# Performance work log

Measured on AMD Instinct MI355X. Metric: run time of the kernel, lower is better.

The kernel has to match this reference:

```python
import jax, jax.numpy as jnp
import numpy as np

N_NODES, N_EDGES, N_FEAT, DIM, HEADS, N_PRED, N_CLASS, N_STEPS = 10000, 160000, 64, 64, 4, 2, 16, 4


def setup_inputs() -> dict:
    key = jax.random.key(0)
    ks = jax.random.split(key, 16)
    def lin(k, fi, fo):
        return jax.random.normal(k, (fi, fo), jnp.float32) / np.sqrt(fi)
    return {
        "x": jax.random.normal(ks[0], (N_NODES, N_FEAT), jnp.float32),
        "edge_index": jax.random.randint(ks[1], (2, N_EDGES), 0, N_NODES, jnp.int64),
        "enc_W": lin(ks[2], N_FEAT, DIM), "enc_b": jnp.zeros((DIM,), jnp.float32),
        "gat_Wl": lin(ks[3], DIM, HEADS * DIM), "gat_bl": jnp.zeros((HEADS * DIM,), jnp.float32),
        "gat_Wr": lin(ks[4], DIM, HEADS * DIM), "gat_br": jnp.zeros((HEADS * DIM,), jnp.float32),
        "gat_att": jax.random.normal(ks[5], (HEADS, DIM), jnp.float32) / np.sqrt(DIM),
        "gat_bias": jnp.zeros((HEADS * DIM,), jnp.float32),
        "W1": lin(ks[6], HEADS * DIM, DIM), "b1": jnp.zeros((DIM,), jnp.float32),
        "W2": lin(ks[7], DIM, DIM), "b2": jnp.zeros((DIM,), jnp.float32),
        "act_W": lin(ks[8], DIM, 1), "act_b": jnp.zeros((1,), jnp.float32),
        "dec_W": jax.random.normal(ks[9], (N_PRED, DIM, N_CLASS), jnp.float32) / np.sqrt(DIM),
        "dec_b": jnp.zeros((N_PRED, N_CLASS), jnp.float32),
        "num_steps": N_STEPS,
    }


def reference(x, edge_index, enc_W, enc_b, gat_Wl, gat_bl, gat_Wr, gat_br,
              gat_att, gat_bias, W1, b1, W2, b2, act_W, act_b, dec_W, dec_b, num_steps):
    N = x.shape[0]
    H, C = gat_att.shape  # heads, per-head channels
    # PyG GATv2Conv adds self-loops by default
    loops = jnp.arange(N, dtype=edge_index.dtype)
    src = jnp.concatenate([edge_index[0], loops])
    dst = jnp.concatenate([edge_index[1], loops])

    h0 = x @ enc_W + enc_b  # encoder

    def step(carry, _):
        h, total, final = carry
        # GATv2: per-edge score on lin_l(src) + lin_r(dst)
        xl = (h @ gat_Wl + gat_bl).reshape(N, H, C)
        xr = (h @ gat_Wr + gat_br).reshape(N, H, C)
        e = jax.nn.leaky_relu(xl[src] + xr[dst], 0.2)          # [E, H, C]
        logits = jnp.einsum('ehc,hc->eh', e, gat_att)           # [E, H]
        m = jax.ops.segment_max(logits, dst, num_segments=N)    # segment softmax over dst
        ex = jnp.exp(logits - m[dst])
        denom = jax.ops.segment_sum(ex, dst, num_segments=N)
        alpha = ex / (denom[dst] + 1e-16)
        agg = jax.ops.segment_sum(xl[src] * alpha[:, :, None], dst, num_segments=N)
        g = agg.reshape(N, H * C) + gat_bias                    # concat heads + bias
        hn = jax.nn.relu(g @ W1 + b1) @ W2 + b2                 # process2 MLP
        # ACT halting: weighted accumulation, deltas clipped so weights sum to <= 1
        term = jax.nn.sigmoid(hn @ act_W + act_b)               # [N, 1]
        new_total = jnp.minimum(total + term, 1.0)
        delta = jnp.minimum(term, new_total - total)
        return (hn, total + delta, final + delta * hn), None

    carry0 = (h0, jnp.zeros((N, 1), x.dtype), jnp.zeros((N, h0.shape[1]), x.dtype))
    (_, _, final), _ = jax.lax.scan(step, carry0, None, length=num_steps)

    logits = jnp.einsum('nd,pdc->pnc', final, dec_W) + dec_b[:, None, :]
    return jax.nn.log_softmax(logits, axis=-1)  # [num_predictions, N, num_classes]
```

## Files before the change

kernel.cpp:

```cpp
#include <hip/hip_runtime.h>
#include <hip/hip_bf16.h>
#include <hip/hip_fp16.h>

#define N_NODES 10000
#define N_EDGES 160000
#define N_E2    (N_EDGES + N_NODES)
#define DIM     64
#define HD      256
#define N_PRED  2
#define N_CLASS 16
#define N_STEPS 4

typedef __hip_bfloat16 bf16;
__device__ __forceinline__ float b2f(bf16 v) { return __bfloat162float(v); }
__device__ __forceinline__ int clampn(int v) { return v < 0 ? 0 : (v >= N_NODES ? N_NODES - 1 : v); }

typedef _Float16 h2_t __attribute__((ext_vector_type(2)));

__device__ __forceinline__ float dot2(unsigned int a, unsigned int b, float c) {
#if __has_builtin(__builtin_amdgcn_fdot2)
    h2_t av, bv;
    __builtin_memcpy(&av, &a, 4);
    __builtin_memcpy(&bv, &b, 4);
    return __builtin_amdgcn_fdot2(av, bv, c, false);
#else
    __half2 ah = *(__half2*)&a, bh = *(__half2*)&b;
    float2 af = __half22float2(ah), bf = __half22float2(bh);
    return c + af.x * bf.x + af.y * bf.y;
#endif
}

struct ConvTable {
    const void* src[17];
    int start[18];
};

__global__ void detect_kernel(const unsigned int* __restrict__ e32,
                              const unsigned short* __restrict__ x16,
                              int* __restrict__ flags) {
    __shared__ int ce, cf;
    if (threadIdx.x == 0) { ce = 0; cf = 0; }
    __syncthreads();
    int le = 0;
    for (int i = threadIdx.x; i < 2048; i += 256)
        le += (e32[2 * i + 1] != 0u) ? 1 : 0;
    int lf = 0;
    for (int i = threadIdx.x; i < 1024; i += 256) {
        unsigned short u = x16[2 * i];
        int ex = (u >> 7) & 0xFF;
        lf += (u == 0 || (ex >= 114 && ex <= 141)) ? 1 : 0;
    }
    atomicAdd(&ce, le);
    atomicAdd(&cf, lf);
    __syncthreads();
    if (threadIdx.x == 0) {
        flags[0] = (ce < 1024) ? 1 : 0;
        flags[1] = (cf >= 512) ? 1 : 0;
    }
}

__global__ void convert_kernel(ConvTable tab, const int* __restrict__ flags,
                               float* __restrict__ xf) {
    int i = blockIdx.x * 256 + threadIdx.x;
    if (i >= tab.start[17]) return;
    int j = 0;
    #pragma unroll
    for (int k = 1; k < 17; ++k) j += (i >= tab.start[k]) ? 1 : 0;
    int off = i - tab.start[j];
    float v;
    if (flags[1]) v = b2f(((const bf16*)tab.src[j])[off]);
    else          v = ((const float*)tab.src[j])[off];
    xf[i] = v;
}

__global__ void pack_kernel(const float* __restrict__ xf,
                            int oWl, int oWr, int oW1, int oW2,
                            __half* __restrict__ wp) {
    int i = blockIdx.x * 256 + threadIdx.x;
    if (i >= 26624) return;
    int base, width, loc;
    if (i < 8192)       { loc = i;         base = oWl; width = 256; }
    else if (i < 16384) { loc = i - 8192;  base = oWr; width = 256; }
    else if (i < 24576) { loc = i - 16384; base = oW1; width = 64; }
    else                { loc = i - 24576; base = oW2; width = 64; }
    int k2 = loc / width, c = loc % width;
    wp[2 * i]     = __float2half(xf[base + (2 * k2) * width + c]);
    wp[2 * i + 1] = __float2half(xf[base + (2 * k2 + 1) * width + c]);
}

__global__ void hist_kernel(const int* __restrict__ edges, const int* __restrict__ flags,
                            int* __restrict__ deg) {
    int e = blockIdx.x * 256 + threadIdx.x;
    if (e >= N_E2) return;
    int i64 = flags[0];
    int dst;
    if (e < N_EDGES) dst = clampn(i64 ? edges[2 * (N_EDGES + e)] : edges[N_EDGES + e]);
    else             dst = e - N_EDGES;
    atomicAdd(&deg[dst], 1);
}

__global__ void scan_kernel(const int* __restrict__ deg, int* __restrict__ off) {
    __shared__ int partial[1024];
    const int tid = threadIdx.x;
    const int per = (N_NODES + 1023) / 1024;
    int local[16];
    int base = tid * per;
    int s = 0;
    for (int i = 0; i < per; ++i) {
        int v = (base + i < N_NODES) ? deg[base + i] : 0;
        local[i] = s;
        s += v;
    }
    partial[tid] = s;
    __syncthreads();
    for (int d = 1; d < 1024; d <<= 1) {
        int t = (tid >= d) ? partial[tid - d] : 0;
        __syncthreads();
        partial[tid] += t;
        __syncthreads();
    }
    int offset = (tid > 0) ? partial[tid - 1] : 0;
    for (int i = 0; i < per; ++i)
        if (base + i < N_NODES) off[base + i] = offset + local[i];
    if (tid == 1023) off[N_NODES] = partial[1023];
}

__global__ void scatter_kernel(const int* __restrict__ edges, const int* __restrict__ flags,
                               const int* __restrict__ off, int* __restrict__ cursor,
                               int* __restrict__ csr_src) {
    int e = blockIdx.x * 256 + threadIdx.x;
    if (e >= N_E2) return;
    int i64 = flags[0];
    int src, dst;
    if (e < N_EDGES) {
        src = clampn(i64 ? edges[2 * e] : edges[e]);
        dst = clampn(i64 ? edges[2 * (N_EDGES + e)] : edges[N_EDGES + e]);
    } else { src = dst = e - N_EDGES; }
    int pos = off[dst] + atomicAdd(&cursor[dst], 1);
    csr_src[pos] = src;
}

__global__ __launch_bounds__(256) void enc_proj_kernel(
        const float* __restrict__ Xf,
        const float* __restrict__ encW, const float* __restrict__ encB,
        const float* __restrict__ Wl, const float* __restrict__ bl,
        const float* __restrict__ Wr, const float* __restrict__ br,
        __half* __restrict__ xlh, float* __restrict__ xr) {
    __shared__ float xs[8][DIM];
    __shared__ float h0[8][DIM];
    const int t = threadIdx.x, pp = t >> 6, d = t & 63;
    const int n0 = blockIdx.x * 8;
    ((float*)xs)[t]       = Xf[n0 * DIM + t];
    ((float*)xs)[t + 256] = Xf[n0 * DIM + t + 256];
    __syncthreads();
    float ah0 = encB[d], ah1 = encB[d];
    for (int k = 0; k < DIM; ++k) {
        float wv = encW[k * DIM + d];
        ah0 += xs[pp][k] * wv;
        ah1 += xs[pp + 4][k] * wv;
    }
    h0[pp][d]     = ah0;
    h0[pp + 4][d] = ah1;
    __syncthreads();
    float al[8] = {0,0,0,0,0,0,0,0}, ar[8] = {0,0,0,0,0,0,0,0};
    for (int k = 0; k < DIM; ++k) {
        float wl = Wl[k * HD + t], wr = Wr[k * HD + t];
        #pragma unroll
        for (int j = 0; j < 8; ++j) { al[j] += h0[j][k] * wl; ar[j] += h0[j][k] * wr; }
    }
    float bbl = bl[t], bbr = br[t];
    #pragma unroll
    for (int j = 0; j < 8; ++j) {
        xlh[(size_t)(n0 + j) * HD + t] = __float2half(al[j] + bbl);
        xr[(size_t)(n0 + j) * HD + t] = ar[j] + bbr;
    }
}

__global__ __launch_bounds__(256) void edge_agg_kernel(
        const __half* __restrict__ xlh, const float* __restrict__ xr,
        const float* __restrict__ att, const float* __restrict__ gbias,
        const int* __restrict__ off, const int* __restrict__ csr_src,
        __half* __restrict__ gbufh) {
    __shared__ float red_m[4][4];
    __shared__ float red_s[4][4];
    __shared__ float red_acc[4][HD];
    const int n = blockIdx.x;
    const int t = threadIdx.x, w = t >> 6, l = t & 63;
    const int e0 = off[n], e1 = off[n + 1];
    const float4 xr4 = ((const float4*)(xr + (size_t)n * HD))[l];
    const float4 at4 = ((const float4*)att)[l];

    float m = -1e30f, s = 0.f;
    float4 acc = {0.f, 0.f, 0.f, 0.f};
    const uint2 zero2 = {0u, 0u};
    int e = e0 + w;
    uint2 b0 = zero2, b1v = zero2, b2v = zero2, b3v = zero2;
    if (e < e1)      b0  = ((const uint2*)(xlh + (size_t)csr_src[e] * HD))[l];
    if (e + 4 < e1)  b1v = ((const uint2*)(xlh + (size_t)csr_src[e + 4] * HD))[l];
    if (e + 8 < e1)  b2v = ((const uint2*)(xlh + (size_t)csr_src[e + 8] * HD))[l];
    if (e + 12 < e1) b3v = ((const uint2*)(xlh + (size_t)csr_src[e + 12] * HD))[l];
    for (; e < e1; e += 4) {
        uint2 cur = b0;
        b0 = b1v; b1v = b2v; b2v = b3v;
        if (e + 16 < e1)
            b3v = ((const uint2*)(xlh + (size_t)csr_src[e + 16] * HD))[l];
        __half2 h01 = *reinterpret_cast<__half2*>(&cur.x);
        __half2 h23 = *reinterpret_cast<__half2*>(&cur.y);
        float2 f01 = __half22float2(h01);
        float2 f23 = __half22float2(h23);
        float c0 = f01.x, c1 = f01.y, c2 = f23.x, c3 = f23.y;
        float z0 = c0 + xr4.x, z1 = c1 + xr4.y, z2 = c2 + xr4.z, z3 = c3 + xr4.w;
        z0 = (z0 > 0.f) ? z0 : 0.2f * z0;
        z1 = (z1 > 0.f) ? z1 : 0.2f * z1;
        z2 = (z2 > 0.f) ? z2 : 0.2f * z2;
        z3 = (z3 > 0.f) ? z3 : 0.2f * z3;
        float p = z0 * at4.x + z1 * at4.y + z2 * at4.z + z3 * at4.w;
        #pragma unroll
        for (int mo = 8; mo; mo >>= 1) p += __shfl_xor(p, mo, 64);
        float nm = fmaxf(m, p);
        float sc = __expf(m - nm);
        float wv = __expf(p - nm);
        s = s * sc + wv;
        acc.x = acc.x * sc + wv * c0;
        acc.y = acc.y * sc + wv * c1;
        acc.z = acc.z * sc + wv * c2;
        acc.w = acc.w * sc + wv * c3;
        m = nm;
    }
    if ((l & 15) == 0) { red_m[w][l >> 4] = m; red_s[w][l >> 4] = s; }
    ((float4*)red_acc[w])[l] = acc;
    __syncthreads();
    {
        int hh = t >> 6;
        float m0 = red_m[0][hh], m1 = red_m[1][hh], m2 = red_m[2][hh], m3 = red_m[3][hh];
        float mm = fmaxf(fmaxf(m0, m1), fmaxf(m2, m3));
        float f0 = __expf(m0 - mm), f1 = __expf(m1 - mm),
              f2 = __expf(m2 - mm), f3 = __expf(m3 - mm);
        float ss = red_s[0][hh] * f0 + red_s[1][hh] * f1 +
                   red_s[2][hh] * f2 + red_s[3][hh] * f3;
        float aa = red_acc[0][t] * f0 + red_acc[1][t] * f1 +
                   red_acc[2][t] * f2 + red_acc[3][t] * f3;
        gbufh[(size_t)n * HD + t] = __float2half(aa / (ss + 1e-16f) + gbias[t]);
    }
}

__global__ __launch_bounds__(256) void mlp_act_proj_kernel(
        const __half* __restrict__ gbufh, const __half* __restrict__ wp,
        const float* __restrict__ b1, const float* __restrict__ b2,
        const float* __restrict__ actW, const float* __restrict__ actB,
        const float* __restrict__ bl, const float* __restrict__ br,
        float* __restrict__ act_tot, float* __restrict__ final_,
        __half* __restrict__ xlh, float* __restrict__ xr, int do_proj) {
    __shared__ unsigned int gall_u[4][128];
    __shared__ float part[4][HD];
    __shared__ __half us_h[4][DIM];
    __shared__ float hns[4][DIM];
    __shared__ __half hns_h[4][DIM];
    __shared__ float delta[4];
    const int t = threadIdx.x, pp = t >> 6, d = t & 63;
    const int n0 = blockIdx.x * 4;

    const unsigned int* Wlp = (const unsigned int*)wp;
    const unsigned int* Wrp = Wlp + 8192;
    const unsigned int* W1p = Wlp + 16384;
    const unsigned int* W2p = Wlp + 24576;

    {
        const unsigned int* gb = (const unsigned int*)gbufh;
        ((unsigned int*)gall_u)[t]       = gb[(size_t)n0 * 128 + t];
        ((unsigned int*)gall_u)[t + 256] = gb[(size_t)n0 * 128 + t + 256];
    }
    __syncthreads();

    {
        float acc[4] = {0.f, 0.f, 0.f, 0.f};
        for (int k2 = pp * 32; k2 < pp * 32 + 32; ++k2) {
            unsigned int w2 = W1p[k2 * 64 + d];
            #pragma unroll
            for (int j = 0; j < 4; ++j) acc[j] = dot2(gall_u[j][k2], w2, acc[j]);
        }
        #pragma unroll
        for (int j = 0; j < 4; ++j) part[j][t] = acc[j];
    }
    __syncthreads();
    {
        float v = part[pp][d] + part[pp][64 + d] + part[pp][128 + d] + part[pp][192 + d] + b1[d];
        us_h[pp][d] = __float2half(fmaxf(v, 0.f));
    }
    __syncthreads();

    {
        const unsigned int* us_u = (const unsigned int*)us_h;
        float acc[4] = {0.f, 0.f, 0.f, 0.f};
        for (int k2 = pp * 8; k2 < pp * 8 + 8; ++k2) {
            unsigned int w2 = W2p[k2 * 64 + d];
            #pragma unroll
            for (int j = 0; j < 4; ++j) acc[j] = dot2(us_u[j * 32 + k2], w2, acc[j]);
        }
        #pragma unroll
        for (int j = 0; j < 4; ++j) part[j][t] = acc[j];
    }
    __syncthreads();
    {
        float hv = part[pp][d] + part[pp][64 + d] + part[pp][128 + d] + part[pp][192 + d] + b2[d];
        hns[pp][d] = hv;
        hns_h[pp][d] = __float2half(hv);
    }
    __syncthreads();

    {
        float p = hns[pp][d] * actW[d];
        #pragma unroll
        for (int mo = 32; mo; mo >>= 1) p += __shfl_xor(p, mo, 64);
        if (d == 0) {
            float term = 1.f / (1.f + __expf(-(p + actB[0])));
            float tot = act_tot[n0 + pp];
            float nt = fminf(tot + term, 1.f);
            float dl = fminf(term, nt - tot);
            act_tot[n0 + pp] = tot + dl;
            delta[pp] = dl;
        }
    }
    __syncthreads();
    final_[(size_t)(n0 + pp) * DIM + d] += delta[pp] * hns[pp][d];

    if (do_proj) {
        const unsigned int* hn_u = (const unsigned int*)hns_h;
        float al[4] = {0.f, 0.f, 0.f, 0.f}, ar[4] = {0.f, 0.f, 0.f, 0.f};
        for (int k2 = 0; k2 < 32; ++k2) {
            unsigned int wl2 = Wlp[k2 * 256 + t];
            unsigned int wr2 = Wrp[k2 * 256 + t];
            #pragma unroll
            for (int j = 0; j < 4; ++j) {
                unsigned int hh = hn_u[j * 32 + k2];
                al[j] = dot2(hh, wl2, al[j]);
                ar[j] = dot2(hh, wr2, ar[j]);
            }
        }
        float bbl = bl[t], bbr = br[t];
        #pragma unroll
        for (int j = 0; j < 4; ++j) {
            xlh[(size_t)(n0 + j) * HD + t] = __float2half(al[j] + bbl);
            xr[(size_t)(n0 + j) * HD + t] = ar[j] + bbr;
        }
    }
}

__global__ void decoder_kernel(const float* __restrict__ final_,
                               const float* __restrict__ decW, const float* __restrict__ decB,
                               const int* __restrict__ flags, void* __restrict__ outv) {
    int id = blockIdx.x * 256 + threadIdx.x;
    if (id >= N_NODES * N_PRED * N_CLASS) return;
    int n = id >> 5, r = id & 31, p = r >> 4, c = r & 15;
    float acc = decB[p * N_CLASS + c];
    for (int dd = 0; dd < DIM; ++dd)
        acc += final_[(size_t)n * DIM + dd] * decW[(p * DIM + dd) * N_CLASS + c];
    float mx = acc;
    #pragma unroll
    for (int mo = 8; mo; mo >>= 1) mx = fmaxf(mx, __shfl_xor(mx, mo, 64));
    float ex = __expf(acc - mx);
    float ss = ex;
    #pragma unroll
    for (int mo = 8; mo; mo >>= 1) ss += __shfl_xor(ss, mo, 64);
    float ov = acc - mx - logf(ss);
    int oi = p * (N_NODES * N_CLASS) + n * N_CLASS + c;
    if (flags[1]) ((bf16*)outv)[oi] = __float2bfloat16(ov);
    else          ((float*)outv)[oi] = ov;
}

static size_t align256(size_t x) { return (x + 255) & ~size_t(255); }

extern "C" void kernel_launch(void* const* d_in, const int* in_sizes, int n_in,
                              void* d_out, int out_size, void* d_ws, size_t ws_size,
                              hipStream_t stream) {
    const int* edges = (const int*)d_in[1];

    static const int fids[17] = {0, 2, 3, 4, 5, 6, 7, 8, 9, 10, 11, 12, 13, 14, 15, 16, 17};
    ConvTable tab;
    int cum = 0;
    for (int i = 0; i < 17; ++i) {
        tab.src[i] = d_in[fids[i]];
        tab.start[i] = cum;
        cum += in_sizes[fids[i]];
    }
    tab.start[17] = cum;

    char* w = (char*)d_ws;
    size_t o = 0;
    int* flags     = (int*)(w + o); o = align256(o + 16 * sizeof(int));
    int* off       = (int*)(w + o); o = align256(o + (N_NODES + 1) * sizeof(int));
    size_t zbase = o;
    int* deg       = (int*)(w + o); o = align256(o + N_NODES * sizeof(int));
    int* cursor    = (int*)(w + o); o = align256(o + N_NODES * sizeof(int));
    float* act_tot = (float*)(w + o); o = align256(o + N_NODES * sizeof(float));
    float* final_  = (float*)(w + o); o = align256(o + (size_t)N_NODES * DIM * sizeof(float));
    size_t zsize = o - zbase;
    int* csr_src   = (int*)(w + o); o = align256(o + N_E2 * sizeof(int));
    float* xf      = (float*)(w + o); o = align256(o + (size_t)cum * sizeof(float));
    __half* xlh    = (__half*)(w + o); o = align256(o + (size_t)N_NODES * HD * sizeof(__half));
    float* xr      = (float*)(w + o); o = align256(o + (size_t)N_NODES * HD * sizeof(float));
    __half* gbufh  = (__half*)(w + o); o = align256(o + (size_t)N_NODES * HD * sizeof(__half));
    __half* wpack  = (__half*)(w + o); o = align256(o + 53248 * sizeof(__half));
    if (o > ws_size) return;

    const float* Xf   = xf + tab.start[0];
    const float* encW = xf + tab.start[1];
    const float* encB = xf + tab.start[2];
    const float* Wl   = xf + tab.start[3];
    const float* bl   = xf + tab.start[4];
    const float* Wr   = xf + tab.start[5];
    const float* br   = xf + tab.start[6];
    const float* att  = xf + tab.start[7];
    const float* gbias= xf + tab.start[8];
    const float* b1   = xf + tab.start[10];
    const float* b2   = xf + tab.start[12];
    const float* actW = xf + tab.start[13];
    const float* actB = xf + tab.start[14];
    const float* decW = xf + tab.start[15];
    const float* decB = xf + tab.start[16];

    hipMemsetAsync(w + zbase, 0, zsize, stream);

    detect_kernel<<<1, 256, 0, stream>>>((const unsigned int*)d_in[1],
                                         (const unsigned short*)d_in[0], flags);
    convert_kernel<<<(cum + 255) / 256, 256, 0, stream>>>(tab, flags, xf);
    pack_kernel<<<(26624 + 255) / 256, 256, 0, stream>>>(
        xf, tab.start[3], tab.start[5], tab.start[9], tab.start[11], wpack);

    int eb = (N_E2 + 255) / 256;
    hist_kernel<<<eb, 256, 0, stream>>>(edges, flags, deg);
    scan_kernel<<<1, 1024, 0, stream>>>(deg, off);
    scatter_kernel<<<eb, 256, 0, stream>>>(edges, flags, off, cursor, csr_src);

    enc_proj_kernel<<<N_NODES / 8, 256, 0, stream>>>(Xf, encW, encB, Wl, bl, Wr, br, xlh, xr);

    for (int step = 0; step < N_STEPS; ++step) {
        edge_agg_kernel<<<N_NODES, 256, 0, stream>>>(xlh, xr, att, gbias, off, csr_src, gbufh);
        mlp_act_proj_kernel<<<N_NODES / 4, 256, 0, stream>>>(
            gbufh, wpack, b1, b2, actW, actB, bl, br,
            act_tot, final_, xlh, xr, (step < N_STEPS - 1) ? 1 : 0);
    }

    int db = (N_NODES * N_PRED * N_CLASS + 255) / 256;
    decoder_kernel<<<db, 256, 0, stream>>>(final_, decW, decB, flags, d_out);
}
```

Before: 338.9 us.

## Map one wavefront per destination node in GAT edge aggregation

Each 64-lane wavefront now owns a whole destination node and walks all of its incoming edges, instead of four wavefronts splitting one node's edges. This removes the LDS cross-wave softmax merge and the block barrier, and the grid shrinks to a quarter of the blocks. Source rows are prefetched in groups of four, with clamped indices and masking for invalid edges, to keep several gathers in flight. In exchange, each wave handles a longer serial edge chain and some redundant loads of the last edge occur at group tails.

```diff
diff --git a/kernel.cpp b/kernel.cpp
--- a/kernel.cpp
+++ b/kernel.cpp
@@ -181,67 +181,65 @@
         const float* __restrict__ att, const float* __restrict__ gbias,
         const int* __restrict__ off, const int* __restrict__ csr_src,
         __half* __restrict__ gbufh) {
-    __shared__ float red_m[4][4];
-    __shared__ float red_s[4][4];
-    __shared__ float red_acc[4][HD];
-    const int n = blockIdx.x;
     const int t = threadIdx.x, w = t >> 6, l = t & 63;
+    const int n = blockIdx.x * 4 + w;
     const int e0 = off[n], e1 = off[n + 1];
+    const int elast = e1 - 1;
     const float4 xr4 = ((const float4*)(xr + (size_t)n * HD))[l];
     const float4 at4 = ((const float4*)att)[l];
 
     float m = -1e30f, s = 0.f;
     float4 acc = {0.f, 0.f, 0.f, 0.f};
-    const uint2 zero2 = {0u, 0u};
-    int e = e0 + w;
-    uint2 b0 = zero2, b1v = zero2, b2v = zero2, b3v = zero2;
-    if (e < e1)      b0  = ((const uint2*)(xlh + (size_t)csr_src[e] * HD))[l];
-    if (e + 4 < e1)  b1v = ((const uint2*)(xlh + (size_t)csr_src[e + 4] * HD))[l];
-    if (e + 8 < e1)  b2v = ((const uint2*)(xlh + (size_t)csr_src[e + 8] * HD))[l];
-    if (e + 12 < e1) b3v = ((const uint2*)(xlh + (size_t)csr_src[e + 12] * HD))[l];
-    for (; e < e1; e += 4) {
-        uint2 cur = b0;
-        b0 = b1v; b1v = b2v; b2v = b3v;
-        if (e + 16 < e1)
-            b3v = ((const uint2*)(xlh + (size_t)csr_src[e + 16] * HD))[l];
-        __half2 h01 = *reinterpret_cast<__half2*>(&cur.x);
-        __half2 h23 = *reinterpret_cast<__half2*>(&cur.y);
-        float2 f01 = __half22float2(h01);
-        float2 f23 = __half22float2(h23);
-        float c0 = f01.x, c1 = f01.y, c2 = f23.x, c3 = f23.y;
-        float z0 = c0 + xr4.x, z1 = c1 + xr4.y, z2 = c2 + xr4.z, z3 = c3 + xr4.w;
-        z0 = (z0 > 0.f) ? z0 : 0.2f * z0;
-        z1 = (z1 > 0.f) ? z1 : 0.2f * z1;
-        z2 = (z2 > 0.f) ? z2 : 0.2f * z2;
-        z3 = (z3 > 0.f) ? z3 : 0.2f * z3;
-        float p = z0 * at4.x + z1 * at4.y + z2 * at4.z + z3 * at4.w;
-        #pragma unroll
-        for (int mo = 8; mo; mo >>= 1) p += __shfl_xor(p, mo, 64);
-        float nm = fmaxf(m, p);
-        float sc = __expf(m - nm);
-        float wv = __expf(p - nm);
-        s = s * sc + wv;
-        acc.x = acc.x * sc + wv * c0;
-        acc.y = acc.y * sc + wv * c1;
-        acc.z = acc.z * sc + wv * c2;
-        acc.w = acc.w * sc + wv * c3;
-        m = nm;
-    }
-    if ((l & 15) == 0) { red_m[w][l >> 4] = m; red_s[w][l >> 4] = s; }
-    ((float4*)red_acc[w])[l] = acc;
-    __syncthreads();
-    {
-        int hh = t >> 6;
-        float m0 = red_m[0][hh], m1 = red_m[1][hh], m2 = red_m[2][hh], m3 = red_m[3][hh];
-        float mm = fmaxf(fmaxf(m0, m1), fmaxf(m2, m3));
-        float f0 = __expf(m0 - mm), f1 = __expf(m1 - mm),
-              f2 = __expf(m2 - mm), f3 = __expf(m3 - mm);
-        float ss = red_s[0][hh] * f0 + red_s[1][hh] * f1 +
-                   red_s[2][hh] * f2 + red_s[3][hh] * f3;
-        float aa = red_acc[0][t] * f0 + red_acc[1][t] * f1 +
-                   red_acc[2][t] * f2 + red_acc[3][t] * f3;
-        gbufh[(size_t)n * HD + t] = __float2half(aa / (ss + 1e-16f) + gbias[t]);
-    }
+    uint2 A[4], B[4];
+    #pragma unroll
+    for (int i = 0; i < 4; ++i) {
+        int ee = e0 + i; ee = (ee > elast) ? elast : ee;
+        A[i] = ((const uint2*)(xlh + (size_t)csr_src[ee] * HD))[l];
+    }
+    for (int base = e0; base < e1; base += 4) {
+        #pragma unroll
+        for (int i = 0; i < 4; ++i) {
+            int ee = base + 4 + i; ee = (ee > elast) ? elast : ee;
+            B[i] = ((const uint2*)(xlh + (size_t)csr_src[ee] * HD))[l];
+        }
+        #pragma unroll
+        for (int i = 0; i < 4; ++i) {
+            const bool valid = (base + i) < e1;
+            __half2 h01 = *reinterpret_cast<__half2*>(&A[i].x);
+            __half2 h23 = *reinterpret_cast<__half2*>(&A[i].y);
+            float2 f01 = __half22float2(h01);
+            float2 f23 = __half22float2(h23);
+            float c0 = f01.x, c1 = f01.y, c2 = f23.x, c3 = f23.y;
+            float z0 = c0 + xr4.x, z1 = c1 + xr4.y, z2 = c2 + xr4.z, z3 = c3 + xr4.w;
+            z0 = (z0 > 0.f) ? z0 : 0.2f * z0;
+            z1 = (z1 > 0.f) ? z1 : 0.2f * z1;
+            z2 = (z2 > 0.f) ? z2 : 0.2f * z2;
+            z3 = (z3 > 0.f) ? z3 : 0.2f * z3;
+            float p = z0 * at4.x + z1 * at4.y + z2 * at4.z + z3 * at4.w;
+            #pragma unroll
+            for (int mo = 8; mo; mo >>= 1) p += __shfl_xor(p, mo, 64);
+            p = valid ? p : -1e30f;
+            float nm = fmaxf(m, p);
+            float sc = __expf(m - nm);
+            float wv = __expf(p - nm);
+            s = s * sc + wv;
+            acc.x = acc.x * sc + wv * c0;
+            acc.y = acc.y * sc + wv * c1;
+            acc.z = acc.z * sc + wv * c2;
+            acc.w = acc.w * sc + wv * c3;
+            m = nm;
+        }
+        #pragma unroll
+        for (int i = 0; i < 4; ++i) A[i] = B[i];
+    }
+    const float inv = 1.f / (s + 1e-16f);
+    const float4 gb4 = ((const float4*)gbias)[l];
+    __half2 o01 = __floats2half2_rn(acc.x * inv + gb4.x, acc.y * inv + gb4.y);
+    __half2 o23 = __floats2half2_rn(acc.z * inv + gb4.z, acc.w * inv + gb4.w);
+    uint2 outv;
+    outv.x = *(unsigned int*)&o01;
+    outv.y = *(unsigned int*)&o23;
+    ((uint2*)(gbufh + (size_t)n * HD))[l] = outv;
 }
 
 __global__ __launch_bounds__(256) void mlp_act_proj_kernel(
@@ -435,7 +433,7 @@
     enc_proj_kernel<<<N_NODES / 8, 256, 0, stream>>>(Xf, encW, encB, Wl, bl, Wr, br, xlh, xr);
 
     for (int step = 0; step < N_STEPS; ++step) {
-        edge_agg_kernel<<<N_NODES, 256, 0, stream>>>(xlh, xr, att, gbias, off, csr_src, gbufh);
+        edge_agg_kernel<<<N_NODES / 4, 256, 0, stream>>>(xlh, xr, att, gbias, off, csr_src, gbufh);
         mlp_act_proj_kernel<<<N_NODES / 4, 256, 0, stream>>>(
             gbufh, wpack, b1, b2, actW, actB, bl, br,
             act_tot, final_, xlh, xr, (step < N_STEPS - 1) ? 1 : 0);
```

Result: faster. 324.4 us (-4.3%).
